# Performance work log

Hardware: AMD Instinct MI355X
Metric: run time of the kernel (lower is better)

## Reference

```python
import jax, jax.numpy as jnp
import numpy as np

RADIUS = 0.25  # module init arg


def _spp(x):
    """Spatial pyramid max pooling over the (K=8, C) plane.
    x: [B, N, 8, C] -> [B, N, 21] (4x4 + 2x2 + 1x1 bins)."""
    B, N, K, C = x.shape
    outs = []
    for h, w in ((4, 4), (2, 2), (1, 1)):
        r = x.reshape(B, N, h, K // h, w, C // w)
        outs.append(r.max(axis=(3, 5)).reshape(B, N, h * w))
    return jnp.concatenate(outs, axis=-1)


def _pointsift_select(xyz, radius):
    """Octant-wise nearest-neighbor selection. xyz: [Bp, N, 3] -> idx [Bp, N, 8]."""
    Bp, N, _ = xyz.shape
    judge = radius * radius
    # diff[b, n, m] = xyz[b, m] - xyz[b, n]  (point m relative to centroid n)
    diff = xyz[:, None, :, :] - xyz[:, :, None, :]          # [Bp, N, N, 3]
    dist = jnp.sum(diff * diff, axis=-1)                     # [Bp, N, N]
    octw = jnp.array([4, 2, 1], dtype=jnp.int32)
    sub = jnp.sum((diff + 1.0).astype(jnp.int32) * octw, -1)  # [Bp, N, N] octant id
    valid = (dist > 1e-10) & (dist < judge)
    eye = jnp.eye(N, dtype=bool)                             # self entry gets judge_dist
    idxs = []
    for i in range(8):
        d_i = jnp.where(valid & (sub == i), dist, 1e10)
        d_i = jnp.where(eye, judge, d_i)
        idxs.append(jnp.argmin(d_i, axis=-1))                # first-min, matches torch
    return jnp.stack(idxs, axis=-1)                          # [Bp, N, 8]


def setup_inputs() -> dict:
    key = jax.random.key(0)
    ks = jax.random.split(key, 7)
    C = 256
    x = jax.random.uniform(ks[0], (2, 2, 2048, 3), dtype=jnp.float32)
    w1 = jax.random.normal(ks[1], (C, 3), dtype=jnp.float32) * 0.05
    b1 = jax.random.normal(ks[2], (C,), dtype=jnp.float32) * 0.05
    w2 = jax.random.normal(ks[3], (C, C), dtype=jnp.float32) * 0.05
    b2 = jax.random.normal(ks[4], (C,), dtype=jnp.float32) * 0.05
    w3 = jax.random.normal(ks[5], (C, C), dtype=jnp.float32) * 0.05
    b3 = jax.random.normal(ks[6], (C,), dtype=jnp.float32) * 0.05
    return {"x": x, "w1": w1, "b1": b1, "w2": w2, "b2": b2, "w3": w3, "b3": b3}


def reference(x, w1, b1, w2, b2, w3, b3):
    B, T, N, _ = x.shape
    xyz = x.reshape(B * T, N, 3)
    idx = _pointsift_select(xyz, RADIUS)                     # [Bp, N, 8]
    b_idx = jnp.arange(B * T)[:, None, None]
    grouped = xyz[b_idx, idx] - xyz[:, :, None, :]           # [Bp, N, 8, 3] relative coords
    # three stacked 1x1 convs (no nonlinearity, per original Sequential)
    h = jnp.einsum('bnkc,oc->bnko', grouped, w1) + b1
    h = jnp.einsum('bnkc,oc->bnko', h, w2) + b2
    h = jnp.einsum('bnkc,oc->bnko', h, w3) + b3              # [Bp, N, 8, C]
    out = _spp(h)                                            # [Bp, N, 21]
    return out.reshape(B, T, N, -1)
```

## Files before the change

kernel.cpp:

```cpp
#include <hip/hip_runtime.h>

#define NPTS 2048
#define CCH  256

#define STARTS_OFF 4096
#define CRD_OFF    8192

template <int CTRL>
__device__ __forceinline__ float dppf(float v) {
    return __int_as_float(__builtin_amdgcn_update_dpp(
        0, __float_as_int(v), CTRL, 0xF, 0xF, true));
}
__device__ __forceinline__ float row16_max(float v) {
    v = fmaxf(v, dppf<0xB1>(v));
    v = fmaxf(v, dppf<0x4E>(v));
    v = fmaxf(v, dppf<0x141>(v));
    v = fmaxf(v, dppf<0x140>(v));
    return v;
}
__device__ __forceinline__ float row16_sum(float v) {
    v += dppf<0xB1>(v);
    v += dppf<0x4E>(v);
    v += dppf<0x141>(v);
    v += dppf<0x140>(v);
    return v;
}
__device__ __forceinline__ float wave_sum(float v) {
    v = row16_sum(v);
    v += __shfl_xor(v, 16, 64);
    v += __shfl_xor(v, 32, 64);
    return v;
}
__device__ __forceinline__ int cell_coord(float v) {
    int c = (int)(v * 4.0f);
    return min(3, max(0, c));
}

__global__ __launch_bounds__(256) void prep_sort_kernel(
    const float* __restrict__ x,
    const float* __restrict__ w1, const float* __restrict__ b1,
    const float* __restrict__ w2, const float* __restrict__ b2,
    const float* __restrict__ w3, const float* __restrict__ b3,
    float* __restrict__ ws, int Bp)
{
    __shared__ float  w3row[2][CCH];
    __shared__ float4 wpart[2][4];
    __shared__ unsigned shist[64];
    __shared__ unsigned scur[64];

    int tid = threadIdx.x;

    if ((int)blockIdx.x < CCH / 2) {
        int o0 = blockIdx.x * 2, c = tid;
        float w3c0 = w3[(o0 + 0) * CCH + c];
        float w3c1 = w3[(o0 + 1) * CCH + c];
        w3row[0][c] = w3c0;
        w3row[1][c] = w3c1;
        __syncthreads();

        float a0 = 0.f, a1 = 0.f, a2 = 0.f, a3 = 0.f;
        float b0 = 0.f, b1p = 0.f, b2p = 0.f, b3p = 0.f;
        const float* w2c = w2 + c;
        for (int k = 0; k < CCH; k += 4) {
            float q0 = w2c[(k + 0) * CCH];
            float q1 = w2c[(k + 1) * CCH];
            float q2 = w2c[(k + 2) * CCH];
            float q3 = w2c[(k + 3) * CCH];
            a0 = fmaf(w3row[0][k + 0], q0, a0);
            a1 = fmaf(w3row[0][k + 1], q1, a1);
            a2 = fmaf(w3row[0][k + 2], q2, a2);
            a3 = fmaf(w3row[0][k + 3], q3, a3);
            b0  = fmaf(w3row[1][k + 0], q0, b0);
            b1p = fmaf(w3row[1][k + 1], q1, b1p);
            b2p = fmaf(w3row[1][k + 2], q2, b2p);
            b3p = fmaf(w3row[1][k + 3], q3, b3p);
        }
        float accA = (a0 + a1) + (a2 + a3);
        float accB = (b0 + b1p) + (b2p + b3p);

        float w1x = w1[c * 3 + 0], w1y = w1[c * 3 + 1], w1z = w1[c * 3 + 2];
        float b1c = b1[c], b2c = b2[c];

        float4 vA = make_float4(accA * w1x, accA * w1y, accA * w1z,
                                fmaf(accA, b1c, w3c0 * b2c));
        float4 vB = make_float4(accB * w1x, accB * w1y, accB * w1z,
                                fmaf(accB, b1c, w3c1 * b2c));
        vA.x = wave_sum(vA.x); vA.y = wave_sum(vA.y);
        vA.z = wave_sum(vA.z); vA.w = wave_sum(vA.w);
        vB.x = wave_sum(vB.x); vB.y = wave_sum(vB.y);
        vB.z = wave_sum(vB.z); vB.w = wave_sum(vB.w);
        if ((c & 63) == 0) {
            wpart[0][c >> 6] = vA;
            wpart[1][c >> 6] = vB;
        }
        __syncthreads();
        if (c < 2) {
            int o = o0 + c;
            float4 p0 = wpart[c][0], p1 = wpart[c][1], p2 = wpart[c][2], p3 = wpart[c][3];
            ws[o * 3 + 0] = (p0.x + p1.x) + (p2.x + p3.x);
            ws[o * 3 + 1] = (p0.y + p1.y) + (p2.y + p3.y);
            ws[o * 3 + 2] = (p0.z + p1.z) + (p2.z + p3.z);
            ws[3 * CCH + o] = (p0.w + p1.w) + (p2.w + p3.w) + b3[o];
        }
        return;
    }

    int b = blockIdx.x - CCH / 2;
    if (b >= Bp) return;
    const float* xb = x + (size_t)b * NPTS * 3;

    if (tid < 64) shist[tid] = 0;
    __syncthreads();

    float a[24];
#pragma unroll
    for (int j = 0; j < 6; ++j)
        *(float4*)(a + 4 * j) = ((const float4*)xb)[tid * 6 + j];

    int cl[8];
#pragma unroll
    for (int k = 0; k < 8; ++k) {
        cl[k] = (cell_coord(a[3 * k + 0]) << 4) |
                (cell_coord(a[3 * k + 1]) << 2) |
                 cell_coord(a[3 * k + 2]);
        atomicAdd(&shist[cl[k]], 1u);
    }
    __syncthreads();

    unsigned* stg = (unsigned*)((char*)ws + STARTS_OFF) + b * 128;
    if (tid < 64) {
        unsigned v = shist[tid];
        unsigned incl = v;
#pragma unroll
        for (int s = 1; s < 64; s <<= 1) {
            unsigned o = __shfl_up(incl, s, 64);
            if (tid >= s) incl += o;
        }
        unsigned excl = incl - v;
        scur[tid] = excl;
        stg[tid] = excl;
        if (tid == 63) stg[64] = NPTS;
    }
    __syncthreads();

    float4* crd = (float4*)((char*)ws + CRD_OFF) + (size_t)b * NPTS;
#pragma unroll
    for (int k = 0; k < 8; ++k) {
        unsigned pos = atomicAdd(&scur[cl[k]], 1u);
        crd[pos] = make_float4(a[3 * k + 0], a[3 * k + 1], a[3 * k + 2],
                               __uint_as_float((unsigned)(8 * tid + k)));
    }
}

__global__ __launch_bounds__(256, 8) void pointsift_kernel(
    const float* __restrict__ x,
    const float* __restrict__ ws,
    float* __restrict__ out)
{
    __shared__ unsigned sstart[65];
    __shared__ unsigned long long soct[4][8];

    int tid = threadIdx.x;
    int batch = blockIdx.x & 3;
    int n0    = (blockIdx.x >> 2) * 4;
    const float* xb = x + (size_t)batch * NPTS * 3;
    const float4* crd = (const float4*)((const char*)ws + CRD_OFF) + (size_t)batch * NPTS;
    const unsigned* stg = (const unsigned*)((const char*)ws + STARTS_OFF) + batch * 128;

    if (tid < 65) sstart[tid] = stg[tid];

    int wave = tid >> 6;
    int lane = tid & 63;
    int n = n0 + wave;

    float3 cpt = *(const float3*)(xb + 3 * n);
    float cx = cpt.x, cy = cpt.y, cz = cpt.z;

    if (lane < 8)
        soct[wave][lane] = (0x7f800000ULL << 32) | (unsigned)n;

    const float4* wsv = (const float4*)ws;
    float4 wa = wsv[lane * 3 + 0];
    float4 wb = wsv[lane * 3 + 1];
    float4 wc = wsv[lane * 3 + 2];
    float4 be = ((const float4*)(ws + 3 * CCH))[lane];

    __syncthreads();

    int ccx = cell_coord(cx), ccy = cell_coord(cy);
    int alo = ccx > 0 ? ccx - 1 : 0;
    int ahi = ccx < 3 ? ccx + 1 : 3;
    int bclo = ccy > 0 ? ccy - 1 : 0;
    int bchi = ccy < 3 ? ccy + 1 : 3;

    for (int a = alo; a <= ahi; ++a) {
        unsigned s0 = sstart[(a << 4) | (bclo << 2)];
        unsigned e0 = sstart[(a << 4) + (bchi << 2) + 4];
        for (unsigned pp = s0 + lane; pp < e0; pp += 64) {
            float4 p = crd[pp];
            float dx = p.x - cx, dy = p.y - cy, dz = p.z - cz;
            float d2 = __fadd_rn(__fadd_rn(__fmul_rn(dx, dx), __fmul_rn(dy, dy)),
                                 __fmul_rn(dz, dz));
            if ((d2 > 1e-10f) && (d2 < 0.0625f)) {
                int oct = 4 * (int)(dx + 1.0f) + 2 * (int)(dy + 1.0f) + (int)(dz + 1.0f);
                unsigned long long key =
                    ((unsigned long long)__float_as_uint(d2) << 32) |
                    __float_as_uint(p.w);
                unsigned long long cur =
                    __hip_atomic_load(&soct[wave][oct], __ATOMIC_RELAXED,
                                      __HIP_MEMORY_SCOPE_WORKGROUP);
                if (key < cur)
                    __hip_atomic_fetch_min(&soct[wave][oct], key,
                                           __ATOMIC_RELAXED,
                                           __HIP_MEMORY_SCOPE_WORKGROUP);
            }
        }
    }

    int nidx[8];
#pragma unroll
    for (int k = 0; k < 8; ++k)
        nidx[k] = (int)(unsigned)soct[wave][k];

    float w[4][3] = {{wa.x, wa.y, wa.z}, {wa.w, wb.x, wb.y},
                     {wb.z, wb.w, wc.x}, {wc.y, wc.z, wc.w}};
    float bev[4] = {be.x, be.y, be.z, be.w};

    float m16[4];
#pragma unroll
    for (int i = 0; i < 4; ++i) m16[i] = -__builtin_inff();
#pragma unroll
    for (int k = 0; k < 8; ++k) {
        float3 p = *(const float3*)(xb + 3 * nidx[k]);
        float gx = p.x - cx, gy = p.y - cy, gz = p.z - cz;
#pragma unroll
        for (int q = 0; q < 4; ++q) {
            float h = fmaf(gx, w[q][0], fmaf(gy, w[q][1], fmaf(gz, w[q][2], bev[q])));
            m16[k >> 1] = fmaxf(m16[k >> 1], h);
        }
    }

    float t[4], u[4];
#pragma unroll
    for (int i = 0; i < 4; ++i) {
        m16[i] = row16_max(m16[i]);
        t[i] = fmaxf(m16[i], __shfl_xor(m16[i], 16, 64));
        u[i] = fmaxf(t[i], __shfl_xor(t[i], 32, 64));
    }

    float* op = out + ((size_t)batch * NPTS + n) * 21;
    if ((lane & 15) == 0) {
        int j = lane >> 4;
#pragma unroll
        for (int i = 0; i < 4; ++i)
            op[i * 4 + j] = m16[i];
    }
    if (lane == 0 || lane == 32) {
        int j2 = lane >> 5;
        op[16 + 0 * 2 + j2] = fmaxf(t[0], t[1]);
        op[16 + 1 * 2 + j2] = fmaxf(t[2], t[3]);
    }
    if (lane == 0) {
        op[20] = fmaxf(fmaxf(u[0], u[1]), fmaxf(u[2], u[3]));
    }
}

extern "C" void kernel_launch(void* const* d_in, const int* in_sizes, int n_in,
                              void* d_out, int out_size, void* d_ws, size_t ws_size,
                              hipStream_t stream) {
    const float* x  = (const float*)d_in[0];
    const float* w1 = (const float*)d_in[1];
    const float* b1 = (const float*)d_in[2];
    const float* w2 = (const float*)d_in[3];
    const float* b2 = (const float*)d_in[4];
    const float* w3 = (const float*)d_in[5];
    const float* b3 = (const float*)d_in[6];
    float* out = (float*)d_out;
    float* ws  = (float*)d_ws;

    int Bp = in_sizes[0] / (NPTS * 3);

    prep_sort_kernel<<<CCH / 2 + Bp, CCH, 0, stream>>>(
        x, w1, b1, w2, b2, w3, b3, ws, Bp);
    pointsift_kernel<<<Bp * (NPTS / 4), 256, 0, stream>>>(x, ws, out);
}
```

Measured before the change: 23.10 us.

## Process four spatially-sorted centroids per wave to share candidate scans

The neighbor-search kernel now gives each wave four consecutive points from the cell-sorted order instead of one original-order point. It scans the union of their neighboring cell ranges once and tests every loaded candidate against all four centroids, so each global load of a candidate is reused four times and the grid shrinks fourfold. The weight-folding blocks in the prep kernel also handle four output channels each instead of two, halving the number of those blocks. The risk is a wider union scan region and more registers per thread, and the launch-bounds occupancy hint has been dropped.

```diff
diff --git a/kernel.cpp b/kernel.cpp
--- a/kernel.cpp
+++ b/kernel.cpp
@@ -43,58 +43,48 @@
     const float* __restrict__ w3, const float* __restrict__ b3,
     float* __restrict__ ws, int Bp)
 {
-    __shared__ float  w3row[2][CCH];
-    __shared__ float4 wpart[2][4];
+    __shared__ float  w3row[4][CCH];
+    __shared__ float4 wpart[4][4];
     __shared__ unsigned shist[64];
     __shared__ unsigned scur[64];
 
     int tid = threadIdx.x;
 
-    if ((int)blockIdx.x < CCH / 2) {
-        int o0 = blockIdx.x * 2, c = tid;
-        float w3c0 = w3[(o0 + 0) * CCH + c];
-        float w3c1 = w3[(o0 + 1) * CCH + c];
-        w3row[0][c] = w3c0;
-        w3row[1][c] = w3c1;
+    if ((int)blockIdx.x < CCH / 4) {
+        int o0 = blockIdx.x * 4, c = tid;
+        float w3c[4];
+#pragma unroll
+        for (int r = 0; r < 4; ++r) {
+            w3c[r] = w3[(o0 + r) * CCH + c];
+            w3row[r][c] = w3c[r];
+        }
         __syncthreads();
 
-        float a0 = 0.f, a1 = 0.f, a2 = 0.f, a3 = 0.f;
-        float b0 = 0.f, b1p = 0.f, b2p = 0.f, b3p = 0.f;
+        float acc[4] = {0.f, 0.f, 0.f, 0.f};
         const float* w2c = w2 + c;
-        for (int k = 0; k < CCH; k += 4) {
+        for (int k = 0; k < CCH; k += 2) {
             float q0 = w2c[(k + 0) * CCH];
             float q1 = w2c[(k + 1) * CCH];
-            float q2 = w2c[(k + 2) * CCH];
-            float q3 = w2c[(k + 3) * CCH];
-            a0 = fmaf(w3row[0][k + 0], q0, a0);
-            a1 = fmaf(w3row[0][k + 1], q1, a1);
-            a2 = fmaf(w3row[0][k + 2], q2, a2);
-            a3 = fmaf(w3row[0][k + 3], q3, a3);
-            b0  = fmaf(w3row[1][k + 0], q0, b0);
-            b1p = fmaf(w3row[1][k + 1], q1, b1p);
-            b2p = fmaf(w3row[1][k + 2], q2, b2p);
-            b3p = fmaf(w3row[1][k + 3], q3, b3p);
-        }
-        float accA = (a0 + a1) + (a2 + a3);
-        float accB = (b0 + b1p) + (b2p + b3p);
+#pragma unroll
+            for (int r = 0; r < 4; ++r) {
+                acc[r] = fmaf(w3row[r][k + 0], q0, acc[r]);
+                acc[r] = fmaf(w3row[r][k + 1], q1, acc[r]);
+            }
+        }
 
         float w1x = w1[c * 3 + 0], w1y = w1[c * 3 + 1], w1z = w1[c * 3 + 2];
         float b1c = b1[c], b2c = b2[c];
 
-        float4 vA = make_float4(accA * w1x, accA * w1y, accA * w1z,
-                                fmaf(accA, b1c, w3c0 * b2c));
-        float4 vB = make_float4(accB * w1x, accB * w1y, accB * w1z,
-                                fmaf(accB, b1c, w3c1 * b2c));
-        vA.x = wave_sum(vA.x); vA.y = wave_sum(vA.y);
-        vA.z = wave_sum(vA.z); vA.w = wave_sum(vA.w);
-        vB.x = wave_sum(vB.x); vB.y = wave_sum(vB.y);
-        vB.z = wave_sum(vB.z); vB.w = wave_sum(vB.w);
-        if ((c & 63) == 0) {
-            wpart[0][c >> 6] = vA;
-            wpart[1][c >> 6] = vB;
+#pragma unroll
+        for (int r = 0; r < 4; ++r) {
+            float4 v = make_float4(acc[r] * w1x, acc[r] * w1y, acc[r] * w1z,
+                                   fmaf(acc[r], b1c, w3c[r] * b2c));
+            v.x = wave_sum(v.x); v.y = wave_sum(v.y);
+            v.z = wave_sum(v.z); v.w = wave_sum(v.w);
+            if ((c & 63) == 0) wpart[r][c >> 6] = v;
         }
         __syncthreads();
-        if (c < 2) {
+        if (c < 4) {
             int o = o0 + c;
             float4 p0 = wpart[c][0], p1 = wpart[c][1], p2 = wpart[c][2], p3 = wpart[c][3];
             ws[o * 3 + 0] = (p0.x + p1.x) + (p2.x + p3.x);
@@ -105,7 +95,7 @@
         return;
     }
 
-    int b = blockIdx.x - CCH / 2;
+    int b = blockIdx.x - CCH / 4;
     if (b >= Bp) return;
     const float* xb = x + (size_t)b * NPTS * 3;
 
@@ -152,32 +142,39 @@
     }
 }
 
-__global__ __launch_bounds__(256, 8) void pointsift_kernel(
+__global__ __launch_bounds__(256) void pointsift_kernel(
     const float* __restrict__ x,
     const float* __restrict__ ws,
     float* __restrict__ out)
 {
     __shared__ unsigned sstart[65];
-    __shared__ unsigned long long soct[4][8];
+    __shared__ unsigned long long soct[4][4][8];
 
     int tid = threadIdx.x;
     int batch = blockIdx.x & 3;
-    int n0    = (blockIdx.x >> 2) * 4;
+    int wave = tid >> 6;
+    int lane = tid & 63;
+    int p0 = (blockIdx.x >> 2) * 16 + wave * 4;
+
     const float* xb = x + (size_t)batch * NPTS * 3;
     const float4* crd = (const float4*)((const char*)ws + CRD_OFF) + (size_t)batch * NPTS;
     const unsigned* stg = (const unsigned*)((const char*)ws + STARTS_OFF) + batch * 128;
 
     if (tid < 65) sstart[tid] = stg[tid];
 
-    int wave = tid >> 6;
-    int lane = tid & 63;
-    int n = n0 + wave;
-
-    float3 cpt = *(const float3*)(xb + 3 * n);
-    float cx = cpt.x, cy = cpt.y, cz = cpt.z;
-
-    if (lane < 8)
-        soct[wave][lane] = (0x7f800000ULL << 32) | (unsigned)n;
+    float4 c4[4];
+    unsigned n_[4];
+#pragma unroll
+    for (int i = 0; i < 4; ++i) {
+        c4[i] = crd[p0 + i];
+        n_[i] = __float_as_uint(c4[i].w);
+    }
+
+    if (lane < 8) {
+#pragma unroll
+        for (int i = 0; i < 4; ++i)
+            soct[wave][i][lane] = (0x7f800000ULL << 32) | n_[i];
+    }
 
     const float4* wsv = (const float4*)ws;
     float4 wa = wsv[lane * 3 + 0];
@@ -187,81 +184,91 @@
 
     __syncthreads();
 
-    int ccx = cell_coord(cx), ccy = cell_coord(cy);
-    int alo = ccx > 0 ? ccx - 1 : 0;
-    int ahi = ccx < 3 ? ccx + 1 : 3;
-    int bclo = ccy > 0 ? ccy - 1 : 0;
-    int bchi = ccy < 3 ? ccy + 1 : 3;
+    int alo = 3, ahi = 0, blo = 3, bhi = 0;
+#pragma unroll
+    for (int i = 0; i < 4; ++i) {
+        int cxl = cell_coord(c4[i].x), cyl = cell_coord(c4[i].y);
+        alo = min(alo, cxl > 0 ? cxl - 1 : 0);
+        ahi = max(ahi, cxl < 3 ? cxl + 1 : 3);
+        blo = min(blo, cyl > 0 ? cyl - 1 : 0);
+        bhi = max(bhi, cyl < 3 ? cyl + 1 : 3);
+    }
 
     for (int a = alo; a <= ahi; ++a) {
-        unsigned s0 = sstart[(a << 4) | (bclo << 2)];
-        unsigned e0 = sstart[(a << 4) + (bchi << 2) + 4];
+        unsigned s0 = sstart[(a << 4) | (blo << 2)];
+        unsigned e0 = sstart[(a << 4) + (bhi << 2) + 4];
         for (unsigned pp = s0 + lane; pp < e0; pp += 64) {
             float4 p = crd[pp];
-            float dx = p.x - cx, dy = p.y - cy, dz = p.z - cz;
-            float d2 = __fadd_rn(__fadd_rn(__fmul_rn(dx, dx), __fmul_rn(dy, dy)),
-                                 __fmul_rn(dz, dz));
-            if ((d2 > 1e-10f) && (d2 < 0.0625f)) {
-                int oct = 4 * (int)(dx + 1.0f) + 2 * (int)(dy + 1.0f) + (int)(dz + 1.0f);
-                unsigned long long key =
-                    ((unsigned long long)__float_as_uint(d2) << 32) |
-                    __float_as_uint(p.w);
-                unsigned long long cur =
-                    __hip_atomic_load(&soct[wave][oct], __ATOMIC_RELAXED,
-                                      __HIP_MEMORY_SCOPE_WORKGROUP);
-                if (key < cur)
-                    __hip_atomic_fetch_min(&soct[wave][oct], key,
-                                           __ATOMIC_RELAXED,
-                                           __HIP_MEMORY_SCOPE_WORKGROUP);
+            unsigned midx = __float_as_uint(p.w);
+#pragma unroll
+            for (int i = 0; i < 4; ++i) {
+                float dx = p.x - c4[i].x, dy = p.y - c4[i].y, dz = p.z - c4[i].z;
+                float d2 = __fadd_rn(__fadd_rn(__fmul_rn(dx, dx), __fmul_rn(dy, dy)),
+                                     __fmul_rn(dz, dz));
+                if ((d2 > 1e-10f) && (d2 < 0.0625f)) {
+                    int oct = 4 * (int)(dx + 1.0f) + 2 * (int)(dy + 1.0f) + (int)(dz + 1.0f);
+                    unsigned long long key =
+                        ((unsigned long long)__float_as_uint(d2) << 32) | midx;
+                    unsigned long long cur =
+                        __hip_atomic_load(&soct[wave][i][oct], __ATOMIC_RELAXED,
+                                          __HIP_MEMORY_SCOPE_WORKGROUP);
+                    if (key < cur)
+                        __hip_atomic_fetch_min(&soct[wave][i][oct], key,
+                                               __ATOMIC_RELAXED,
+                                               __HIP_MEMORY_SCOPE_WORKGROUP);
+                }
             }
         }
     }
-
-    int nidx[8];
-#pragma unroll
-    for (int k = 0; k < 8; ++k)
-        nidx[k] = (int)(unsigned)soct[wave][k];
 
     float w[4][3] = {{wa.x, wa.y, wa.z}, {wa.w, wb.x, wb.y},
                      {wb.z, wb.w, wc.x}, {wc.y, wc.z, wc.w}};
     float bev[4] = {be.x, be.y, be.z, be.w};
 
-    float m16[4];
-#pragma unroll
-    for (int i = 0; i < 4; ++i) m16[i] = -__builtin_inff();
-#pragma unroll
-    for (int k = 0; k < 8; ++k) {
-        float3 p = *(const float3*)(xb + 3 * nidx[k]);
-        float gx = p.x - cx, gy = p.y - cy, gz = p.z - cz;
+#pragma unroll
+    for (int i = 0; i < 4; ++i) {
+        int nidx[8];
+#pragma unroll
+        for (int k = 0; k < 8; ++k)
+            nidx[k] = (int)(unsigned)soct[wave][i][k];
+
+        float m16[4];
+#pragma unroll
+        for (int q = 0; q < 4; ++q) m16[q] = -__builtin_inff();
+#pragma unroll
+        for (int k = 0; k < 8; ++k) {
+            float3 p = *(const float3*)(xb + 3 * nidx[k]);
+            float gx = p.x - c4[i].x, gy = p.y - c4[i].y, gz = p.z - c4[i].z;
+#pragma unroll
+            for (int q = 0; q < 4; ++q) {
+                float h = fmaf(gx, w[q][0], fmaf(gy, w[q][1], fmaf(gz, w[q][2], bev[q])));
+                m16[k >> 1] = fmaxf(m16[k >> 1], h);
+            }
+        }
+
+        float t[4], u[4];
 #pragma unroll
         for (int q = 0; q < 4; ++q) {
-            float h = fmaf(gx, w[q][0], fmaf(gy, w[q][1], fmaf(gz, w[q][2], bev[q])));
-            m16[k >> 1] = fmaxf(m16[k >> 1], h);
-        }
-    }
-
-    float t[4], u[4];
-#pragma unroll
-    for (int i = 0; i < 4; ++i) {
-        m16[i] = row16_max(m16[i]);
-        t[i] = fmaxf(m16[i], __shfl_xor(m16[i], 16, 64));
-        u[i] = fmaxf(t[i], __shfl_xor(t[i], 32, 64));
-    }
-
-    float* op = out + ((size_t)batch * NPTS + n) * 21;
-    if ((lane & 15) == 0) {
-        int j = lane >> 4;
-#pragma unroll
-        for (int i = 0; i < 4; ++i)
-            op[i * 4 + j] = m16[i];
-    }
-    if (lane == 0 || lane == 32) {
-        int j2 = lane >> 5;
-        op[16 + 0 * 2 + j2] = fmaxf(t[0], t[1]);
-        op[16 + 1 * 2 + j2] = fmaxf(t[2], t[3]);
-    }
-    if (lane == 0) {
-        op[20] = fmaxf(fmaxf(u[0], u[1]), fmaxf(u[2], u[3]));
+            m16[q] = row16_max(m16[q]);
+            t[q] = fmaxf(m16[q], __shfl_xor(m16[q], 16, 64));
+            u[q] = fmaxf(t[q], __shfl_xor(t[q], 32, 64));
+        }
+
+        float* op = out + ((size_t)batch * NPTS + n_[i]) * 21;
+        if ((lane & 15) == 0) {
+            int j = lane >> 4;
+#pragma unroll
+            for (int q = 0; q < 4; ++q)
+                op[q * 4 + j] = m16[q];
+        }
+        if (lane == 0 || lane == 32) {
+            int j2 = lane >> 5;
+            op[16 + 0 * 2 + j2] = fmaxf(t[0], t[1]);
+            op[16 + 1 * 2 + j2] = fmaxf(t[2], t[3]);
+        }
+        if (lane == 0) {
+            op[20] = fmaxf(fmaxf(u[0], u[1]), fmaxf(u[2], u[3]));
+        }
     }
 }
 
@@ -280,7 +287,7 @@
 
     int Bp = in_sizes[0] / (NPTS * 3);
 
-    prep_sort_kernel<<<CCH / 2 + Bp, CCH, 0, stream>>>(
+    prep_sort_kernel<<<CCH / 4 + Bp, CCH, 0, stream>>>(
         x, w1, b1, w2, b2, w3, b3, ws, Bp);
-    pointsift_kernel<<<Bp * (NPTS / 4), 256, 0, stream>>>(x, ws, out);
-}
+    pointsift_kernel<<<Bp * (NPTS / 16), 256, 0, stream>>>(x, ws, out);
+}
```

After: 30.43 us. +31.7%, slower.
